# Optimization experiments

Measured on AMD Instinct MI355X. Metric: run time of the kernel, lower is better.

## Reference

```python
import jax, jax.numpy as jnp
import numpy as np

B, C, H, W = 256, 2048, 24, 12
K = 6  # num_parts


def setup_inputs() -> dict:
    key = jax.random.key(0)
    kx, kc = jax.random.split(key)
    x = jax.random.normal(kx, (B, C, H, W), dtype=jnp.float32)
    clusters = jax.random.normal(kc, (K, C), dtype=jnp.float32)
    return {"x": x, "clusters": clusters}


def reference(x, clusters):
    b, c, h, w = x.shape
    k = clusters.shape[0]
    # [B, C, H, W] -> [B, N, C], N = H*W
    xf = x.reshape(b, c, h * w).transpose(0, 2, 1)
    x_norm = jnp.sum(xf * xf, axis=-1, keepdims=True)          # [B, N, 1]
    c_norm = jnp.sum(clusters * clusters, axis=-1)             # [K]
    dist = x_norm + c_norm[None, None, :] - 2.0 * jnp.einsum('bnc,kc->bnk', xf, clusters)
    dist = jnp.nan_to_num(dist)                                # dist[dist != dist] = 0
    assign = jnp.argmin(dist, axis=-1)                         # [B, N]
    # per-cluster mean via one-hot segment-sum (vectorized scatter-mean)
    onehot = jax.nn.one_hot(assign, k, dtype=xf.dtype)         # [B, N, K]
    sums = jnp.einsum('bnk,bnc->bkc', onehot, xf)              # [B, K, C]
    counts = jnp.sum(onehot, axis=1)                           # [B, K]
    # empty cluster -> NaN mean in torch -> replaced by 0 via remove_nan
    means = jnp.where(counts[..., None] > 0,
                      sums / jnp.maximum(counts, 1.0)[..., None],
                      0.0)                                     # [B, K, C]
    return means.transpose(0, 2, 1)                            # [B, C, K]
```

## Files before the change

### kernel.cpp

```cpp
#include <hip/hip_runtime.h>


#define NB 256
#define NC 2048
#define NN 288
#define NK 6
#define NT 1024
#define NJ 72
#define NP 14

__global__ __launch_bounds__(NT) void cluster_kernel(
    const float* __restrict__ x,
    const float* __restrict__ cl,
    float* __restrict__ out)
{
    __shared__ double part[4][NN][NK];
    __shared__ double cnorm_s[NK];
    __shared__ unsigned assign_u[NN / 4];
    __shared__ int counts[NK];
    __shared__ float inv_s[NK];

    const int tid = threadIdx.x;
    const int b = blockIdx.x;
    const float* xb = x + (size_t)b * (size_t)(NC * NN);

    if (tid < NK) counts[tid] = 0;

    const int j = tid % NJ;
    const int p = tid / NJ;
    const int w = tid >> 6;
    const int lane = tid & 63;

    if (w < NK) {
        const int k = w;
        double s = 0.0;
#pragma unroll 4
        for (int c = lane; c < NC; c += 64) {
            double d = (double)cl[k * NC + c];
            s += d * d;
        }
#pragma unroll
        for (int off = 1; off < 64; off <<= 1) s += __shfl_xor(s, off, 64);
        if (lane == 0) cnorm_s[k] = s;
    }

    double acc[4][NK];
#pragma unroll
    for (int r = 0; r < 4; ++r)
#pragma unroll
        for (int k = 0; k < NK; ++k) acc[r][k] = 0.0;

    if (p < NP) {
#pragma unroll 2
        for (int c = p; c < NC; c += NP) {
            float4 v = *(const float4*)(xb + (size_t)c * NN + 4 * j);
            double vx = v.x, vy = v.y, vz = v.z, vw = v.w;
#pragma unroll
            for (int k = 0; k < NK; ++k) {
                double ck = (double)cl[k * NC + c];
                acc[0][k] += vx * ck;
                acc[1][k] += vy * ck;
                acc[2][k] += vz * ck;
                acc[3][k] += vw * ck;
            }
        }
    }

    if (p < 4) {
#pragma unroll
        for (int r = 0; r < 4; ++r)
#pragma unroll
            for (int k = 0; k < NK; ++k) part[p][4 * j + r][k] = acc[r][k];
    }
    __syncthreads();
    if (p >= 4 && p < 8) {
#pragma unroll
        for (int r = 0; r < 4; ++r)
#pragma unroll
            for (int k = 0; k < NK; ++k) part[p - 4][4 * j + r][k] += acc[r][k];
    }
    __syncthreads();
    if (p >= 8 && p < 12) {
#pragma unroll
        for (int r = 0; r < 4; ++r)
#pragma unroll
            for (int k = 0; k < NK; ++k) part[p - 8][4 * j + r][k] += acc[r][k];
    }
    __syncthreads();
    if (p >= 12 && p < NP) {
#pragma unroll
        for (int r = 0; r < 4; ++r)
#pragma unroll
            for (int k = 0; k < NK; ++k) part[p - 12][4 * j + r][k] += acc[r][k];
    }
    __syncthreads();

    if (tid < NN) {
        double best = 1e300;
        int bi = 0;
#pragma unroll
        for (int k = 0; k < NK; ++k) {
            double d = 0.0;
#pragma unroll
            for (int q = 0; q < 4; ++q) d += part[q][tid][k];
            double sc = cnorm_s[k] - 2.0 * d;
            if (sc < best) { best = sc; bi = k; }
        }
        ((unsigned char*)assign_u)[tid] = (unsigned char)bi;
        atomicAdd(&counts[bi], 1);
    }
    __syncthreads();
    if (tid < NK) inv_s[tid] = counts[tid] > 0 ? 1.0f / (float)counts[tid] : 0.0f;
    __syncthreads();

    const int sub = lane >> 4;
    const int sl = lane & 15;
    float* outb = out + (size_t)b * (size_t)(NC * NK);

    for (int cb = 4 * w; cb < NC; cb += 4 * (NT / 64)) {
        const int c = cb + sub;
        const float* row = xb + (size_t)c * NN;
        float a[NK];
#pragma unroll
        for (int k = 0; k < NK; ++k) a[k] = 0.f;

#pragma unroll
        for (int t = 0; t < 4; ++t) {
            const int g = sl + 16 * t;
            float4 v = *(const float4*)(row + 4 * g);
            unsigned am = assign_u[g];
            float vv[4] = {v.x, v.y, v.z, v.w};
#pragma unroll
            for (int r = 0; r < 4; ++r) {
                int ar = (int)((am >> (8 * r)) & 0xffu);
#pragma unroll
                for (int k = 0; k < NK; ++k) a[k] += (ar == k) ? vv[r] : 0.f;
            }
        }
        if (sl < 8) {
            const int g = 64 + sl;
            float4 v = *(const float4*)(row + 4 * g);
            unsigned am = assign_u[g];
            float vv[4] = {v.x, v.y, v.z, v.w};
#pragma unroll
            for (int r = 0; r < 4; ++r) {
                int ar = (int)((am >> (8 * r)) & 0xffu);
#pragma unroll
                for (int k = 0; k < NK; ++k) a[k] += (ar == k) ? vv[r] : 0.f;
            }
        }

#pragma unroll
        for (int off = 1; off < 16; off <<= 1) {
#pragma unroll
            for (int k = 0; k < NK; ++k) a[k] += __shfl_xor(a[k], off, 64);
        }

        if (sl < NK) {
            float val = a[0];
            if (sl == 1) val = a[1];
            else if (sl == 2) val = a[2];
            else if (sl == 3) val = a[3];
            else if (sl == 4) val = a[4];
            else if (sl == 5) val = a[5];
            outb[(size_t)c * NK + sl] = val * inv_s[sl];
        }
    }
}

extern "C" void kernel_launch(void* const* d_in, const int* in_sizes, int n_in,
                              void* d_out, int out_size, void* d_ws, size_t ws_size,
                              hipStream_t stream) {
    const float* x = (const float*)d_in[0];
    const float* clusters = (const float*)d_in[1];
    float* out = (float*)d_out;
    hipLaunchKernelGGL(cluster_kernel, dim3(NB), dim3(NT), 0, stream,
                       x, clusters, out);
}
```

Measured before the change: 892.7 us.

## Switch distance dot-products to fp32 with LDS-staged clusters and prefetched loads

The x·cluster dot products now accumulate in fp32 instead of fp64. The cluster matrix is staged once into shared memory, and the work is remapped so each wave walks a strided set of channels across all 288 positions. The next group of x rows is register-prefetched so loads overlap with the FMAs. The partial-sum layout is transposed and padded to reduce LDS bank conflicts. The aim is to remove slow fp64 arithmetic and repeated global cluster loads, at the cost of reduced precision, which could flip argmin results for near-tied distances.

```diff
diff --git a/kernel.cpp b/kernel.cpp
--- a/kernel.cpp
+++ b/kernel.cpp
@@ -6,92 +6,154 @@
 #define NN 288
 #define NK 6
 #define NT 1024
-#define NJ 72
-#define NP 14
 
 __global__ __launch_bounds__(NT) void cluster_kernel(
     const float* __restrict__ x,
     const float* __restrict__ cl,
     float* __restrict__ out)
 {
-    __shared__ double part[4][NN][NK];
+    __shared__ float cls[NK * NC];
+    __shared__ float part[4][NK][NN + 1];
     __shared__ double cnorm_s[NK];
     __shared__ unsigned assign_u[NN / 4];
     __shared__ int counts[NK];
     __shared__ float inv_s[NK];
 
     const int tid = threadIdx.x;
+    const int w = tid >> 6;
+    const int lane = tid & 63;
     const int b = blockIdx.x;
     const float* xb = x + (size_t)b * (size_t)(NC * NN);
 
     if (tid < NK) counts[tid] = 0;
 
-    const int j = tid % NJ;
-    const int p = tid / NJ;
-    const int w = tid >> 6;
-    const int lane = tid & 63;
-
+    {
+        const float4* src = (const float4*)cl;
+        float4* dst = (float4*)cls;
+#pragma unroll
+        for (int t = 0; t < 3; ++t) dst[tid + NT * t] = src[tid + NT * t];
+    }
     if (w < NK) {
-        const int k = w;
         double s = 0.0;
 #pragma unroll 4
         for (int c = lane; c < NC; c += 64) {
-            double d = (double)cl[k * NC + c];
+            double d = (double)cl[w * NC + c];
             s += d * d;
         }
 #pragma unroll
         for (int off = 1; off < 64; off <<= 1) s += __shfl_xor(s, off, 64);
-        if (lane == 0) cnorm_s[k] = s;
-    }
-
-    double acc[4][NK];
+        if (lane == 0) cnorm_s[w] = s;
+    }
+    __syncthreads();
+
+    float acc[4][NK];
+    float acct[NK];
 #pragma unroll
     for (int r = 0; r < 4; ++r)
 #pragma unroll
-        for (int k = 0; k < NK; ++k) acc[r][k] = 0.0;
-
-    if (p < NP) {
-#pragma unroll 2
-        for (int c = p; c < NC; c += NP) {
-            float4 v = *(const float4*)(xb + (size_t)c * NN + 4 * j);
-            double vx = v.x, vy = v.y, vz = v.z, vw = v.w;
+        for (int k = 0; k < NK; ++k) acc[r][k] = 0.f;
+#pragma unroll
+    for (int k = 0; k < NK; ++k) acct[k] = 0.f;
+
+    const bool tl = lane < 32;
+    float4 buf[4];
+    float buft[4] = {0.f, 0.f, 0.f, 0.f};
+
+#pragma unroll
+    for (int u = 0; u < 4; ++u) {
+        const int c = w + 16 * u;
+        buf[u] = *(const float4*)(xb + (size_t)c * NN + 4 * lane);
+    }
+    if (tl) {
+#pragma unroll
+        for (int u = 0; u < 4; ++u) {
+            const int c = w + 16 * u;
+            buft[u] = xb[(size_t)c * NN + 256 + lane];
+        }
+    }
+
+    for (int t = 0; t < 32; ++t) {
+        float4 cur[4];
+        float curt[4];
+#pragma unroll
+        for (int u = 0; u < 4; ++u) { cur[u] = buf[u]; curt[u] = buft[u]; }
+
+        if (t < 31) {
+#pragma unroll
+            for (int u = 0; u < 4; ++u) {
+                const int c = w + 64 * (t + 1) + 16 * u;
+                buf[u] = *(const float4*)(xb + (size_t)c * NN + 4 * lane);
+            }
+            if (tl) {
+#pragma unroll
+                for (int u = 0; u < 4; ++u) {
+                    const int c = w + 64 * (t + 1) + 16 * u;
+                    buft[u] = xb[(size_t)c * NN + 256 + lane];
+                }
+            }
+        }
+
+#pragma unroll
+        for (int u = 0; u < 4; ++u) {
+            const int c = w + 64 * t + 16 * u;
+            float ck[NK];
+#pragma unroll
+            for (int k = 0; k < NK; ++k) ck[k] = cls[k * NC + c];
 #pragma unroll
             for (int k = 0; k < NK; ++k) {
-                double ck = (double)cl[k * NC + c];
-                acc[0][k] += vx * ck;
-                acc[1][k] += vy * ck;
-                acc[2][k] += vz * ck;
-                acc[3][k] += vw * ck;
-            }
-        }
-    }
-
-    if (p < 4) {
-#pragma unroll
-        for (int r = 0; r < 4; ++r)
-#pragma unroll
-            for (int k = 0; k < NK; ++k) part[p][4 * j + r][k] = acc[r][k];
-    }
-    __syncthreads();
-    if (p >= 4 && p < 8) {
-#pragma unroll
-        for (int r = 0; r < 4; ++r)
-#pragma unroll
-            for (int k = 0; k < NK; ++k) part[p - 4][4 * j + r][k] += acc[r][k];
-    }
-    __syncthreads();
-    if (p >= 8 && p < 12) {
-#pragma unroll
-        for (int r = 0; r < 4; ++r)
-#pragma unroll
-            for (int k = 0; k < NK; ++k) part[p - 8][4 * j + r][k] += acc[r][k];
-    }
-    __syncthreads();
-    if (p >= 12 && p < NP) {
-#pragma unroll
-        for (int r = 0; r < 4; ++r)
-#pragma unroll
-            for (int k = 0; k < NK; ++k) part[p - 12][4 * j + r][k] += acc[r][k];
+                acc[0][k] += cur[u].x * ck[k];
+                acc[1][k] += cur[u].y * ck[k];
+                acc[2][k] += cur[u].z * ck[k];
+                acc[3][k] += cur[u].w * ck[k];
+                acct[k]  += curt[u] * ck[k];
+            }
+        }
+    }
+
+    const int q = w & 3;
+    const int stage = w >> 2;
+    if (stage == 0) {
+#pragma unroll
+        for (int r = 0; r < 4; ++r)
+#pragma unroll
+            for (int k = 0; k < NK; ++k) part[q][k][4 * lane + r] = acc[r][k];
+        if (tl) {
+#pragma unroll
+            for (int k = 0; k < NK; ++k) part[q][k][256 + lane] = acct[k];
+        }
+    }
+    __syncthreads();
+    if (stage == 1) {
+#pragma unroll
+        for (int r = 0; r < 4; ++r)
+#pragma unroll
+            for (int k = 0; k < NK; ++k) part[q][k][4 * lane + r] += acc[r][k];
+        if (tl) {
+#pragma unroll
+            for (int k = 0; k < NK; ++k) part[q][k][256 + lane] += acct[k];
+        }
+    }
+    __syncthreads();
+    if (stage == 2) {
+#pragma unroll
+        for (int r = 0; r < 4; ++r)
+#pragma unroll
+            for (int k = 0; k < NK; ++k) part[q][k][4 * lane + r] += acc[r][k];
+        if (tl) {
+#pragma unroll
+            for (int k = 0; k < NK; ++k) part[q][k][256 + lane] += acct[k];
+        }
+    }
+    __syncthreads();
+    if (stage == 3) {
+#pragma unroll
+        for (int r = 0; r < 4; ++r)
+#pragma unroll
+            for (int k = 0; k < NK; ++k) part[q][k][4 * lane + r] += acc[r][k];
+        if (tl) {
+#pragma unroll
+            for (int k = 0; k < NK; ++k) part[q][k][256 + lane] += acct[k];
+        }
     }
     __syncthreads();
 
@@ -100,9 +162,8 @@
         int bi = 0;
 #pragma unroll
         for (int k = 0; k < NK; ++k) {
-            double d = 0.0;
-#pragma unroll
-            for (int q = 0; q < 4; ++q) d += part[q][tid][k];
+            double d = (double)part[0][k][tid] + (double)part[1][k][tid]
+                     + (double)part[2][k][tid] + (double)part[3][k][tid];
             double sc = cnorm_s[k] - 2.0 * d;
             if (sc < best) { best = sc; bi = k; }
         }
```

Result: no change. 893.1 us (+0.0%).
